# Kernel optimization log

Measured on AMD Instinct MI355X. Metric: run time of the kernel, lower is better.

## Reference

```python
import jax, jax.numpy as jnp
import numpy as np

N_NODES = 100000
N_EDGES = 1600000
D_IN = 64
D_OUT = 64
K_PLUS = 3
ALPHA = 0.5
EXPONENT = -0.25


def _dir_norm_edge_weights(row, col, n, exponent):
    # directed_norm: D_out^exp A D_in^exp, zero-degree -> 0 weight
    ones = jnp.ones(row.shape[0], dtype=jnp.float32)
    out_deg = jax.ops.segment_sum(ones, row, num_segments=n)
    in_deg = jax.ops.segment_sum(ones, col, num_segments=n)
    out_inv = jnp.where(out_deg > 0, jnp.power(jnp.maximum(out_deg, 1.0), exponent), 0.0)
    in_inv = jnp.where(in_deg > 0, jnp.power(jnp.maximum(in_deg, 1.0), exponent), 0.0)
    return out_inv[row] * in_inv[col]


def _spmm(w, x, out_idx, gather_idx, n):
    # y[out_idx] += w * x[gather_idx]
    return jax.ops.segment_sum(w[:, None] * x[gather_idx], out_idx, num_segments=n)


def setup_inputs() -> dict:
    key = jax.random.key(0)
    ks = jax.random.split(key, 7)
    x_real = jax.random.normal(ks[0], (N_NODES, D_IN), dtype=jnp.float32)
    x_imag = jax.random.normal(ks[1], (N_NODES, D_IN), dtype=jnp.float32)
    edge_index = jax.random.randint(ks[2], (2, N_EDGES), 0, N_NODES, dtype=jnp.int32)
    s = 1.0 / np.sqrt(D_IN)
    W_real = jax.random.normal(ks[3], (K_PLUS, D_OUT, D_IN), dtype=jnp.float32) * s
    b_real = jax.random.normal(ks[4], (K_PLUS, D_OUT), dtype=jnp.float32) * s
    W_imag = jax.random.normal(ks[5], (K_PLUS, D_OUT, D_IN), dtype=jnp.float32) * s
    b_imag = jax.random.normal(ks[6], (K_PLUS, D_OUT), dtype=jnp.float32) * s
    return {"x_real": x_real, "x_imag": x_imag, "edge_index": edge_index,
            "W_real": W_real, "b_real": b_real, "W_imag": W_imag, "b_imag": b_imag}


def reference(x_real, x_imag, edge_index, W_real, b_real, W_imag, b_imag):
    n = x_real.shape[0]
    row, col = edge_index[0], edge_index[1]
    # adj_norm edge weights; adj_t_norm weights are identical scalars per edge
    # (in/out degrees swap under transpose), only the scatter direction differs.
    w = _dir_norm_edge_weights(row, col, n, EXPONENT)

    y_real = _spmm(w, x_real, row, col, n)    # adj_norm @ x_real
    y_imag = _spmm(w, x_imag, row, col, n)    # adj_norm @ x_imag
    y_real_t = _spmm(w, x_real, col, row, n)  # adj_t_norm @ x_real
    y_imag_t = _spmm(w, x_imag, col, row, n)  # adj_t_norm @ x_imag

    def lin_r(y):  # [K, N, O] per-order real linear
        return jnp.einsum('nd,kod->kno', y, W_real) + b_real[:, None, :]

    def lin_i(y):
        return jnp.einsum('nd,kod->kno', y, W_imag) + b_imag[:, None, :]

    coeffs = (0.5 ** jnp.arange(K_PLUS, dtype=jnp.float32))[:, None, None]  # exp penalty, i=0 -> 1

    lr_yr, li_yr = lin_r(y_real), lin_i(y_real)
    lr_yi, li_yi = lin_r(y_imag), lin_i(y_imag)
    lr_yrt, li_yrt = lin_r(y_real_t), lin_i(y_real_t)
    lr_yit, li_yit = lin_r(y_imag_t), lin_i(y_imag_t)

    sum_real_s2d = jnp.sum((lr_yr - li_yi) * coeffs, axis=0)
    sum_imag_s2d = jnp.sum((li_yr + lr_yi) * coeffs, axis=0)
    sum_real_d2s = jnp.sum((lr_yrt - li_yit) * coeffs, axis=0)
    # NOTE: faithful to original source, which uses y_real (not y_real_t) here.
    sum_imag_d2s = jnp.sum((li_yr + lr_yit) * coeffs, axis=0)

    total_real = ALPHA * sum_real_s2d + (1.0 - ALPHA) * sum_real_d2s
    total_imag = ALPHA * sum_imag_s2d + (1.0 - ALPHA) * sum_imag_d2s
    return total_real, total_imag
```

## Files before the change

kernel.cpp:

```cpp
#include <hip/hip_runtime.h>
#include <hip/hip_fp16.h>


constexpr int D = 64;
constexpr int GSC = 500;
constexpr int SLOTSZ = 8192;

typedef _Float16 f16x8 __attribute__((ext_vector_type(8)));
typedef float f32x4 __attribute__((ext_vector_type(4)));

__device__ __forceinline__ float2 h2_to_f2(uint p) {
  __half2 h = *(__half2*)&p;
  return __half22float2(h);
}

__global__ __launch_bounds__(1024) void prep_kernel(
    const float* __restrict__ Wr, const float* __restrict__ br,
    const float* __restrict__ Wi, const float* __restrict__ bi,
    uint4* __restrict__ Bfrag, float* __restrict__ cR, float* __restrict__ cI,
    int* __restrict__ Ccur, int NBUK) {
  __shared__ uint sWh[4096];
  int t = threadIdx.x;
  for (int i = t; i < 4096; i += 1024) {
    int o = i >> 6, d = i & 63;
    float wr = Wr[i] + 0.5f * Wr[4096 + i] + 0.25f * Wr[8192 + i];
    float wi = Wi[i] + 0.5f * Wi[4096 + i] + 0.25f * Wi[8192 + i];
    __half2 h = __floats2half2_rn(wr, wi);
    sWh[d * 64 + o] = *(uint*)&h;
  }
  if (t < 64) {
    float brv = br[t] + 0.5f * br[64 + t] + 0.25f * br[128 + t];
    float biv = bi[t] + 0.5f * bi[64 + t] + 0.25f * bi[128 + t];
    cR[t] = brv - biv;
    cI[t] = brv + biv;
  }
  for (int i = t; i < 2 * NBUK; i += 1024) {
    int b = (i < NBUK) ? i : (i - NBUK);
    Ccur[i << 4] = b * SLOTSZ;
  }
  __syncthreads();
  for (int tt = t; tt < 2048; tt += 1024) {
    int ln = tt & 63, fr = tt >> 6;
    int mat = fr >> 4, kt = (fr >> 2) & 3, nt = fr & 3;
    int o = (ln & 15) + 16 * nt;
    int k0 = 8 * (ln >> 4) + 32 * kt;
    uint wbits[4];
#pragma unroll
    for (int jj = 0; jj < 4; ++jj) {
      float vv[2];
#pragma unroll
      for (int s = 0; s < 2; ++s) {
        int k = k0 + 2 * jj + s;
        float2 wrwi = h2_to_f2(sWh[(k & 63) * 64 + o]);
        vv[s] = (k < 64) ? wrwi.x : (mat ? wrwi.y : -wrwi.y);
      }
      __half2 hh = __floats2half2_rn(vv[0], vv[1]);
      wbits[jj] = *(uint*)&hh;
    }
    Bfrag[tt] = make_uint4(wbits[0], wbits[1], wbits[2], wbits[3]);
  }
}

__global__ __launch_bounds__(256) void part_scatter(
    const int* __restrict__ row, const int* __restrict__ col,
    int* __restrict__ Ccur,
    uint* __restrict__ pout, uint* __restrict__ pin, int E, int NBUK, int CH) {
  __shared__ int co[512], ci[512];
  int t = threadIdx.x, g = blockIdx.x;
  co[t] = 0;
  co[t + 256] = 0;
  ci[t] = 0;
  ci[t + 256] = 0;
  __syncthreads();
  int e0 = g * CH, e1 = min(E, e0 + CH);
  int g0 = e0 >> 2, g1 = (e1 + 3) >> 2;
  for (int gi = g0 + t; gi < g1; gi += 256) {
    int4 r4 = ((const int4*)row)[gi];
    int4 c4 = ((const int4*)col)[gi];
    atomicAdd(&co[r4.x >> 8], 1);
    atomicAdd(&co[r4.y >> 8], 1);
    atomicAdd(&co[r4.z >> 8], 1);
    atomicAdd(&co[r4.w >> 8], 1);
    atomicAdd(&ci[c4.x >> 8], 1);
    atomicAdd(&ci[c4.y >> 8], 1);
    atomicAdd(&ci[c4.z >> 8], 1);
    atomicAdd(&ci[c4.w >> 8], 1);
  }
  __syncthreads();
  for (int i = t; i < NBUK; i += 256) {
    int c = co[i];
    co[i] = c ? atomicAdd(&Ccur[i << 4], c) : 0;
    c = ci[i];
    ci[i] = c ? atomicAdd(&Ccur[(NBUK + i) << 4], c) : 0;
  }
  __syncthreads();
  for (int gi = g0 + t; gi < g1; gi += 256) {
    int4 r4 = ((const int4*)row)[gi];
    int4 c4 = ((const int4*)col)[gi];
#define SCAT1(R, C)                                          \
  {                                                          \
    int po = atomicAdd(&co[(R) >> 8], 1);                    \
    pout[po] = ((uint)((R) & 255) << 17) | (uint)(C);        \
    int pi = atomicAdd(&ci[(C) >> 8], 1);                    \
    pin[pi] = ((uint)((C) & 255) << 17) | (uint)(R);         \
  }
    SCAT1(r4.x, c4.x);
    SCAT1(r4.y, c4.y);
    SCAT1(r4.z, c4.z);
    SCAT1(r4.w, c4.w);
#undef SCAT1
  }
}

__global__ __launch_bounds__(256) void build_kernel(
    const uint* __restrict__ pout, const uint* __restrict__ pin,
    const int* __restrict__ Ccur,
    int2* __restrict__ ofsp_out, int2* __restrict__ ofsp_in,
    float* __restrict__ inv_out, float* __restrict__ inv_in,
    uint* __restrict__ idx_out, uint* __restrict__ idx_in, int NBUK, int N) {
  const uint* p = blockIdx.y ? pin : pout;
  int2* ofsp = blockIdx.y ? ofsp_in : ofsp_out;
  float* inv = blockIdx.y ? inv_in : inv_out;
  uint* idx = blockIdx.y ? idx_in : idx_out;
  __shared__ int ld[256], cur[256];
  __shared__ int ws[4];
  int t = threadIdx.x, b = blockIdx.x;
  ld[t] = 0;
  __syncthreads();
  int s = b * SLOTSZ;
  int e = Ccur[((blockIdx.y ? NBUK : 0) + b) << 4];
  int j = s + t;
  for (; j + 768 < e; j += 1024) {
    uint p0 = p[j], p1 = p[j + 256], p2 = p[j + 512], p3 = p[j + 768];
    atomicAdd(&ld[p0 >> 17], 1);
    atomicAdd(&ld[p1 >> 17], 1);
    atomicAdd(&ld[p2 >> 17], 1);
    atomicAdd(&ld[p3 >> 17], 1);
  }
  for (; j < e; j += 256) atomicAdd(&ld[p[j] >> 17], 1);
  __syncthreads();
  int d = ld[t];
  int lane = t & 63, wv = t >> 6, sc = d;
#pragma unroll
  for (int off = 1; off < 64; off <<= 1) {
    int u = __shfl_up(sc, off);
    if (lane >= off) sc += u;
  }
  if (lane == 63) ws[wv] = sc;
  __syncthreads();
  int wbase = 0;
#pragma unroll
  for (int w = 0; w < 4; ++w)
    if (w < wv) wbase += ws[w];
  int start = s + wbase + sc - d;
  cur[t] = start;
  int n = (b << 8) + t;
  if (n < N) {
    ofsp[n] = make_int2(start, start + d);
    inv[n] = d ? rsqrtf(sqrtf((float)d)) : 0.0f;
  }
  __syncthreads();
  j = s + t;
#define FILL1(PK)                                  \
  {                                                \
    int pos = atomicAdd(&cur[(PK) >> 17], 1);      \
    idx[pos] = (PK) & 0x1FFFFu;                    \
  }
  for (; j + 768 < e; j += 1024) {
    uint p0 = p[j], p1 = p[j + 256], p2 = p[j + 512], p3 = p[j + 768];
    FILL1(p0);
    FILL1(p1);
    FILL1(p2);
    FILL1(p3);
  }
  for (; j < e; j += 256) {
    uint pk = p[j];
    FILL1(pk);
  }
#undef FILL1
}


__global__ void pack_kernel(const float* __restrict__ xr, const float* __restrict__ xi,
                            uint* __restrict__ xp, int total4) {
  int i = blockIdx.x * blockDim.x + threadIdx.x;
  if (i < total4) {
    float4 a = ((const float4*)xr)[i];
    float4 b = ((const float4*)xi)[i];
    __half2 h;
    uint4 o;
    h = __floats2half2_rn(a.x, b.x); o.x = *(uint*)&h;
    h = __floats2half2_rn(a.y, b.y); o.y = *(uint*)&h;
    h = __floats2half2_rn(a.z, b.z); o.z = *(uint*)&h;
    h = __floats2half2_rn(a.w, b.w); o.w = *(uint*)&h;
    ((uint4*)xp)[i] = o;
  }
}

__global__ __launch_bounds__(256) void gather_kernel(
    const uint4* __restrict__ xp4,
    const uint* __restrict__ idx_out, const uint* __restrict__ idx_in,
    const int2* __restrict__ ofsp_out, const int2* __restrict__ ofsp_in,
    const float* __restrict__ inv_out, const float* __restrict__ inv_in,
    uint* __restrict__ Apack, int N) {
  int wv = threadIdx.x >> 6;
  int lane = threadIdx.x & 63;
  int sub = lane >> 4;
  int q = lane & 15;
  int wid = blockIdx.x * 4 + wv;
  int nw = gridDim.x * 4;
  for (int n = wid; n < N; n += nw) {
    float4 u1 = {0, 0, 0, 0}, s1 = {0, 0, 0, 0};
    float4 v2 = {0, 0, 0, 0}, s2 = {0, 0, 0, 0};
#define ACC(P, SC, U, S)                                                \
  {                                                                     \
    float2 a0 = h2_to_f2((P).x), a1 = h2_to_f2((P).y);                  \
    float2 a2 = h2_to_f2((P).z), a3 = h2_to_f2((P).w);                  \
    U.x += SC * a0.x; S.x += SC * a0.y; U.y += SC * a1.x; S.y += SC * a1.y; \
    U.z += SC * a2.x; S.z += SC * a2.y; U.w += SC * a3.x; S.w += SC * a3.y; \
  }
    {
      int2 se = ofsp_out[n];
      int lo = se.x, hi = se.y;
      int len8 = (hi - lo) & ~7;
      int j = lo;
      for (; j < lo + len8; j += 8) {
        uint e0 = idx_out[j + sub];
        uint e1 = idx_out[j + 4 + sub];
        uint4 p0 = xp4[(size_t)e0 * 16 + q];
        uint4 p1 = xp4[(size_t)e1 * 16 + q];
        float sc0 = inv_in[e0], sc1 = inv_in[e1];
        ACC(p0, sc0, u1, s1);
        ACC(p1, sc1, u1, s1);
      }
      for (; j < hi; j += 4) {
        if (j + sub < hi) {
          uint e0 = idx_out[j + sub];
          uint4 p0 = xp4[(size_t)e0 * 16 + q];
          float sc0 = inv_in[e0];
          ACC(p0, sc0, u1, s1);
        }
      }
    }
    {
      int2 se = ofsp_in[n];
      int lo = se.x, hi = se.y;
      int len8 = (hi - lo) & ~7;
      int j = lo;
      for (; j < lo + len8; j += 8) {
        uint e0 = idx_in[j + sub];
        uint e1 = idx_in[j + 4 + sub];
        uint4 p0 = xp4[(size_t)e0 * 16 + q];
        uint4 p1 = xp4[(size_t)e1 * 16 + q];
        float sc0 = inv_out[e0], sc1 = inv_out[e1];
        ACC(p0, sc0, v2, s2);
        ACC(p1, sc1, v2, s2);
      }
      for (; j < hi; j += 4) {
        if (j + sub < hi) {
          uint e0 = idx_in[j + sub];
          uint4 p0 = xp4[(size_t)e0 * 16 + q];
          float sc0 = inv_out[e0];
          ACC(p0, sc0, v2, s2);
        }
      }
    }
#undef ACC
#pragma unroll
    for (int m = 16; m < 64; m <<= 1) {
      u1.x += __shfl_xor(u1.x, m); u1.y += __shfl_xor(u1.y, m);
      u1.z += __shfl_xor(u1.z, m); u1.w += __shfl_xor(u1.w, m);
      s1.x += __shfl_xor(s1.x, m); s1.y += __shfl_xor(s1.y, m);
      s1.z += __shfl_xor(s1.z, m); s1.w += __shfl_xor(s1.w, m);
      v2.x += __shfl_xor(v2.x, m); v2.y += __shfl_xor(v2.y, m);
      v2.z += __shfl_xor(v2.z, m); v2.w += __shfl_xor(v2.w, m);
      s2.x += __shfl_xor(s2.x, m); s2.y += __shfl_xor(s2.y, m);
      s2.z += __shfl_xor(s2.z, m); s2.w += __shfl_xor(s2.w, m);
    }
    if (sub == 0) {
      float io = inv_out[n], ii = inv_in[n];
      float4 uu = make_float4(io * u1.x, io * u1.y, io * u1.z, io * u1.w);
      float4 vv = make_float4(ii * v2.x, ii * v2.y, ii * v2.z, ii * v2.w);
      float4 ss = make_float4(io * s1.x + ii * s2.x, io * s1.y + ii * s2.y,
                              io * s1.z + ii * s2.z, io * s1.w + ii * s2.w);
      uint* base = Apack + (size_t)n * 96 + 2 * q;
      __half2 h;
      uint2 w;
      h = __floats2half2_rn(0.5f * (uu.x + vv.x), 0.5f * (uu.y + vv.y)); w.x = *(uint*)&h;
      h = __floats2half2_rn(0.5f * (uu.z + vv.z), 0.5f * (uu.w + vv.w)); w.y = *(uint*)&h;
      *(uint2*)base = w;
      h = __floats2half2_rn(0.5f * ss.x, 0.5f * ss.y); w.x = *(uint*)&h;
      h = __floats2half2_rn(0.5f * ss.z, 0.5f * ss.w); w.y = *(uint*)&h;
      *(uint2*)(base + 32) = w;
      h = __floats2half2_rn(uu.x, uu.y); w.x = *(uint*)&h;
      h = __floats2half2_rn(uu.z, uu.w); w.y = *(uint*)&h;
      *(uint2*)(base + 64) = w;
    }
  }
}

__global__ __launch_bounds__(256) void gemm_kernel(
    const ushort* __restrict__ Apack, const uint4* __restrict__ Bfrag,
    const float* __restrict__ cR, const float* __restrict__ cI,
    float* __restrict__ out_real, float* __restrict__ out_imag, int N) {
  __shared__ uint4 sB[2048];
  for (int i = threadIdx.x; i < 2048; i += 256) sB[i] = Bfrag[i];
  __syncthreads();
  int lane = threadIdx.x & 63, wv = threadIdx.x >> 6;
  int l15 = lane & 15, l4 = lane >> 4;
  float bR[4], bI[4];
#pragma unroll
  for (int nt = 0; nt < 4; ++nt) {
    bR[nt] = cR[l15 + 16 * nt];
    bI[nt] = cI[l15 + 16 * nt];
  }
  int tiles = (N + 15) >> 4;
  int gw = blockIdx.x * 4 + wv, nw = gridDim.x * 4;
  for (int tt = gw; tt < tiles; tt += nw) {
    int n0 = tt << 4;
    int arow = min(n0 + l15, N - 1);
    const ushort* ap = Apack + (size_t)arow * 192 + 8 * l4;
    f16x8 a[6];
#pragma unroll
    for (int kt = 0; kt < 6; ++kt) a[kt] = *(const f16x8*)(ap + 32 * kt);
    f32x4 cr[4], ci[4];
#pragma unroll
    for (int nt = 0; nt < 4; ++nt) {
      cr[nt] = (f32x4){0.f, 0.f, 0.f, 0.f};
      ci[nt] = (f32x4){0.f, 0.f, 0.f, 0.f};
    }
#pragma unroll
    for (int kt = 0; kt < 4; ++kt) {
#pragma unroll
      for (int nt = 0; nt < 4; ++nt) {
        f16x8 b0 = *(const f16x8*)&sB[(kt * 4 + nt) * 64 + lane];
        cr[nt] = __builtin_amdgcn_mfma_f32_16x16x32_f16(a[kt], b0, cr[nt], 0, 0, 0);
        f16x8 b1 = *(const f16x8*)&sB[(16 + kt * 4 + nt) * 64 + lane];
        ci[nt] = __builtin_amdgcn_mfma_f32_16x16x32_f16(a[kt + 2], b1, ci[nt], 0, 0, 0);
      }
    }
#pragma unroll
    for (int nt = 0; nt < 4; ++nt) {
#pragma unroll
      for (int r = 0; r < 4; ++r) {
        int node = n0 + 4 * l4 + r;
        if (node < N) {
          out_real[(size_t)node * 64 + l15 + 16 * nt] = cr[nt][r] + bR[nt];
          out_imag[(size_t)node * 64 + l15 + 16 * nt] = ci[nt][r] + bI[nt];
        }
      }
    }
  }
}

extern "C" void kernel_launch(void* const* d_in, const int* in_sizes, int n_in,
                              void* d_out, int out_size, void* d_ws, size_t ws_size,
                              hipStream_t stream) {
  const float* x_real = (const float*)d_in[0];
  const float* x_imag = (const float*)d_in[1];
  const int* edge = (const int*)d_in[2];
  const float* W_real = (const float*)d_in[3];
  const float* b_real = (const float*)d_in[4];
  const float* W_imag = (const float*)d_in[5];
  const float* b_imag = (const float*)d_in[6];

  const int N = in_sizes[0] / D;
  const int E = in_sizes[2] / 2;
  const int* row = edge;
  const int* col = edge + E;

  const int NBUK = (N + 255) >> 8;
  const int CH = ((E / GSC + 3) & ~3);
  const size_t SLOTS = (size_t)NBUK * SLOTSZ;

  uint* xp       = (uint*)d_ws;
  uint* idx_out  = xp + (size_t)N * D;
  uint* idx_in   = idx_out + SLOTS;
  uint* Apack    = idx_in + SLOTS;
  uint* pout     = Apack;
  uint* pin      = pout + SLOTS;
  uint4* Bfrag   = (uint4*)(Apack + (size_t)N * 96);
  int* Ccur      = (int*)(Bfrag + 2048);
  int2* ofsp_out = (int2*)(Ccur + 2 * NBUK * 16);
  int2* ofsp_in  = ofsp_out + N;
  float* inv_out = (float*)(ofsp_in + N);
  float* inv_in  = inv_out + N;
  float* cR      = inv_in + N;
  float* cI      = cR + 64;

  float* out_real = (float*)d_out;
  float* out_imag = out_real + (size_t)N * D;

  prep_kernel<<<1, 1024, 0, stream>>>(W_real, b_real, W_imag, b_imag,
                                      Bfrag, cR, cI, Ccur, NBUK);

  pack_kernel<<<(N * 16 + 255) / 256, 256, 0, stream>>>(x_real, x_imag, xp, N * 16);

  part_scatter<<<GSC, 256, 0, stream>>>(row, col, Ccur, pout, pin, E, NBUK, CH);

  build_kernel<<<dim3(NBUK, 2), 256, 0, stream>>>(pout, pin, Ccur,
                                                  ofsp_out, ofsp_in,
                                                  inv_out, inv_in,
                                                  idx_out, idx_in, NBUK, N);

  gather_kernel<<<4096, 256, 0, stream>>>((const uint4*)xp, idx_out, idx_in,
                                          ofsp_out, ofsp_in, inv_out, inv_in,
                                          Apack, N);
  gemm_kernel<<<1568, 256, 0, stream>>>((const ushort*)Apack, Bfrag, cR, cI,
                                        out_real, out_imag, N);
}
```

Measured before the change: 331.3 us.

## Fuse prep/pack/scatter kernels and embed neighbor scale into edge index

Merges weight prep, fp16 packing and the partition scatter into one heterogeneous launch, with Ccur zeroed by a memset and bucket-relative counters. The build step is split into an offsets kernel and a fill kernel. The fill kernel stores each neighbor's fp16 inverse-degree scale in the upper bits of the index word, so the gather no longer does a separate random load of inv_in/inv_out per edge. The cost is one extra kernel launch, a random scale lookup moved into the fill pass, and fp16 precision for the edge scales.

```diff
diff --git a/kernel.cpp b/kernel.cpp
--- a/kernel.cpp
+++ b/kernel.cpp
@@ -5,6 +5,7 @@
 constexpr int D = 64;
 constexpr int GSC = 500;
 constexpr int SLOTSZ = 8192;
+constexpr int PREPB = 8;
 
 typedef _Float16 f16x8 __attribute__((ext_vector_type(8)));
 typedef float f32x4 __attribute__((ext_vector_type(4)));
@@ -14,89 +15,50 @@
   return __half22float2(h);
 }
 
-__global__ __launch_bounds__(1024) void prep_kernel(
+__global__ __launch_bounds__(256) void phase1_kernel(
+    const int* __restrict__ row, const int* __restrict__ col,
+    int* __restrict__ Ccur, uint* __restrict__ pout, uint* __restrict__ pin,
+    const float* __restrict__ xr, const float* __restrict__ xi,
+    uint* __restrict__ xp,
     const float* __restrict__ Wr, const float* __restrict__ br,
     const float* __restrict__ Wi, const float* __restrict__ bi,
     uint4* __restrict__ Bfrag, float* __restrict__ cR, float* __restrict__ cI,
-    int* __restrict__ Ccur, int NBUK) {
-  __shared__ uint sWh[4096];
-  int t = threadIdx.x;
-  for (int i = t; i < 4096; i += 1024) {
-    int o = i >> 6, d = i & 63;
-    float wr = Wr[i] + 0.5f * Wr[4096 + i] + 0.25f * Wr[8192 + i];
-    float wi = Wi[i] + 0.5f * Wi[4096 + i] + 0.25f * Wi[8192 + i];
-    __half2 h = __floats2half2_rn(wr, wi);
-    sWh[d * 64 + o] = *(uint*)&h;
-  }
-  if (t < 64) {
-    float brv = br[t] + 0.5f * br[64 + t] + 0.25f * br[128 + t];
-    float biv = bi[t] + 0.5f * bi[64 + t] + 0.25f * bi[128 + t];
-    cR[t] = brv - biv;
-    cI[t] = brv + biv;
-  }
-  for (int i = t; i < 2 * NBUK; i += 1024) {
-    int b = (i < NBUK) ? i : (i - NBUK);
-    Ccur[i << 4] = b * SLOTSZ;
-  }
-  __syncthreads();
-  for (int tt = t; tt < 2048; tt += 1024) {
-    int ln = tt & 63, fr = tt >> 6;
-    int mat = fr >> 4, kt = (fr >> 2) & 3, nt = fr & 3;
-    int o = (ln & 15) + 16 * nt;
-    int k0 = 8 * (ln >> 4) + 32 * kt;
-    uint wbits[4];
-#pragma unroll
-    for (int jj = 0; jj < 4; ++jj) {
-      float vv[2];
-#pragma unroll
-      for (int s = 0; s < 2; ++s) {
-        int k = k0 + 2 * jj + s;
-        float2 wrwi = h2_to_f2(sWh[(k & 63) * 64 + o]);
-        vv[s] = (k < 64) ? wrwi.x : (mat ? wrwi.y : -wrwi.y);
-      }
-      __half2 hh = __floats2half2_rn(vv[0], vv[1]);
-      wbits[jj] = *(uint*)&hh;
-    }
-    Bfrag[tt] = make_uint4(wbits[0], wbits[1], wbits[2], wbits[3]);
-  }
-}
-
-__global__ __launch_bounds__(256) void part_scatter(
-    const int* __restrict__ row, const int* __restrict__ col,
-    int* __restrict__ Ccur,
-    uint* __restrict__ pout, uint* __restrict__ pin, int E, int NBUK, int CH) {
-  __shared__ int co[512], ci[512];
-  int t = threadIdx.x, g = blockIdx.x;
-  co[t] = 0;
-  co[t + 256] = 0;
-  ci[t] = 0;
-  ci[t + 256] = 0;
-  __syncthreads();
-  int e0 = g * CH, e1 = min(E, e0 + CH);
-  int g0 = e0 >> 2, g1 = (e1 + 3) >> 2;
-  for (int gi = g0 + t; gi < g1; gi += 256) {
-    int4 r4 = ((const int4*)row)[gi];
-    int4 c4 = ((const int4*)col)[gi];
-    atomicAdd(&co[r4.x >> 8], 1);
-    atomicAdd(&co[r4.y >> 8], 1);
-    atomicAdd(&co[r4.z >> 8], 1);
-    atomicAdd(&co[r4.w >> 8], 1);
-    atomicAdd(&ci[c4.x >> 8], 1);
-    atomicAdd(&ci[c4.y >> 8], 1);
-    atomicAdd(&ci[c4.z >> 8], 1);
-    atomicAdd(&ci[c4.w >> 8], 1);
-  }
-  __syncthreads();
-  for (int i = t; i < NBUK; i += 256) {
-    int c = co[i];
-    co[i] = c ? atomicAdd(&Ccur[i << 4], c) : 0;
-    c = ci[i];
-    ci[i] = c ? atomicAdd(&Ccur[(NBUK + i) << 4], c) : 0;
-  }
-  __syncthreads();
-  for (int gi = g0 + t; gi < g1; gi += 256) {
-    int4 r4 = ((const int4*)row)[gi];
-    int4 c4 = ((const int4*)col)[gi];
+    int E, int NBUK, int CH, int NPACK, int total4) {
+  __shared__ uint smem[4096];
+  int t = threadIdx.x, bid = blockIdx.x;
+  if (bid < GSC) {
+    int* co = (int*)smem;
+    int* ci = co + 512;
+    co[t] = 0;
+    co[t + 256] = 0;
+    ci[t] = 0;
+    ci[t + 256] = 0;
+    __syncthreads();
+    int e0 = bid * CH, e1 = min(E, e0 + CH);
+    int g0 = e0 >> 2, g1 = (e1 + 3) >> 2;
+    for (int gi = g0 + t; gi < g1; gi += 256) {
+      int4 r4 = ((const int4*)row)[gi];
+      int4 c4 = ((const int4*)col)[gi];
+      atomicAdd(&co[r4.x >> 8], 1);
+      atomicAdd(&co[r4.y >> 8], 1);
+      atomicAdd(&co[r4.z >> 8], 1);
+      atomicAdd(&co[r4.w >> 8], 1);
+      atomicAdd(&ci[c4.x >> 8], 1);
+      atomicAdd(&ci[c4.y >> 8], 1);
+      atomicAdd(&ci[c4.z >> 8], 1);
+      atomicAdd(&ci[c4.w >> 8], 1);
+    }
+    __syncthreads();
+    for (int i = t; i < NBUK; i += 256) {
+      int c = co[i];
+      co[i] = c ? i * SLOTSZ + atomicAdd(&Ccur[i << 4], c) : 0;
+      c = ci[i];
+      ci[i] = c ? i * SLOTSZ + atomicAdd(&Ccur[(NBUK + i) << 4], c) : 0;
+    }
+    __syncthreads();
+    for (int gi = g0 + t; gi < g1; gi += 256) {
+      int4 r4 = ((const int4*)row)[gi];
+      int4 c4 = ((const int4*)col)[gi];
 #define SCAT1(R, C)                                          \
   {                                                          \
     int po = atomicAdd(&co[(R) >> 8], 1);                    \
@@ -104,31 +66,80 @@
     int pi = atomicAdd(&ci[(C) >> 8], 1);                    \
     pin[pi] = ((uint)((C) & 255) << 17) | (uint)(R);         \
   }
-    SCAT1(r4.x, c4.x);
-    SCAT1(r4.y, c4.y);
-    SCAT1(r4.z, c4.z);
-    SCAT1(r4.w, c4.w);
+      SCAT1(r4.x, c4.x);
+      SCAT1(r4.y, c4.y);
+      SCAT1(r4.z, c4.z);
+      SCAT1(r4.w, c4.w);
 #undef SCAT1
-  }
-}
-
-__global__ __launch_bounds__(256) void build_kernel(
+    }
+  } else if (bid < GSC + NPACK) {
+    int i = (bid - GSC) * 256 + t;
+    if (i < total4) {
+      float4 a = ((const float4*)xr)[i];
+      float4 b = ((const float4*)xi)[i];
+      __half2 h;
+      uint4 o;
+      h = __floats2half2_rn(a.x, b.x); o.x = *(uint*)&h;
+      h = __floats2half2_rn(a.y, b.y); o.y = *(uint*)&h;
+      h = __floats2half2_rn(a.z, b.z); o.z = *(uint*)&h;
+      h = __floats2half2_rn(a.w, b.w); o.w = *(uint*)&h;
+      ((uint4*)xp)[i] = o;
+    }
+  } else {
+    int pb = bid - GSC - NPACK;
+    uint* sWh = smem;
+    for (int i = t; i < 4096; i += 256) {
+      int o = i >> 6, d = i & 63;
+      float wr = Wr[i] + 0.5f * Wr[4096 + i] + 0.25f * Wr[8192 + i];
+      float wi = Wi[i] + 0.5f * Wi[4096 + i] + 0.25f * Wi[8192 + i];
+      __half2 h = __floats2half2_rn(wr, wi);
+      sWh[d * 64 + o] = *(uint*)&h;
+    }
+    if (pb == 0 && t < 64) {
+      float brv = br[t] + 0.5f * br[64 + t] + 0.25f * br[128 + t];
+      float biv = bi[t] + 0.5f * bi[64 + t] + 0.25f * bi[128 + t];
+      cR[t] = brv - biv;
+      cI[t] = brv + biv;
+    }
+    __syncthreads();
+    int tt = pb * 256 + t;
+    int ln = tt & 63, fr = tt >> 6;
+    int mat = fr >> 4, kt = (fr >> 2) & 3, nt = fr & 3;
+    int o = (ln & 15) + 16 * nt;
+    int k0 = 8 * (ln >> 4) + 32 * kt;
+    uint wbits[4];
+#pragma unroll
+    for (int jj = 0; jj < 4; ++jj) {
+      float vv[2];
+#pragma unroll
+      for (int s = 0; s < 2; ++s) {
+        int k = k0 + 2 * jj + s;
+        float2 wrwi = h2_to_f2(sWh[(k & 63) * 64 + o]);
+        vv[s] = (k < 64) ? wrwi.x : (mat ? wrwi.y : -wrwi.y);
+      }
+      __half2 hh = __floats2half2_rn(vv[0], vv[1]);
+      wbits[jj] = *(uint*)&hh;
+    }
+    Bfrag[tt] = make_uint4(wbits[0], wbits[1], wbits[2], wbits[3]);
+  }
+}
+
+__global__ __launch_bounds__(256) void offsets_kernel(
     const uint* __restrict__ pout, const uint* __restrict__ pin,
     const int* __restrict__ Ccur,
     int2* __restrict__ ofsp_out, int2* __restrict__ ofsp_in,
     float* __restrict__ inv_out, float* __restrict__ inv_in,
-    uint* __restrict__ idx_out, uint* __restrict__ idx_in, int NBUK, int N) {
+    int NBUK, int N) {
   const uint* p = blockIdx.y ? pin : pout;
   int2* ofsp = blockIdx.y ? ofsp_in : ofsp_out;
   float* inv = blockIdx.y ? inv_in : inv_out;
-  uint* idx = blockIdx.y ? idx_in : idx_out;
-  __shared__ int ld[256], cur[256];
+  __shared__ int ld[256];
   __shared__ int ws[4];
   int t = threadIdx.x, b = blockIdx.x;
   ld[t] = 0;
   __syncthreads();
   int s = b * SLOTSZ;
-  int e = Ccur[((blockIdx.y ? NBUK : 0) + b) << 4];
+  int e = s + Ccur[((blockIdx.y ? NBUK : 0) + b) << 4];
   int j = s + t;
   for (; j + 768 < e; j += 1024) {
     uint p0 = p[j], p1 = p[j + 256], p2 = p[j + 512], p3 = p[j + 768];
@@ -153,19 +164,38 @@
   for (int w = 0; w < 4; ++w)
     if (w < wv) wbase += ws[w];
   int start = s + wbase + sc - d;
-  cur[t] = start;
   int n = (b << 8) + t;
   if (n < N) {
     ofsp[n] = make_int2(start, start + d);
     inv[n] = d ? rsqrtf(sqrtf((float)d)) : 0.0f;
   }
+}
+
+__global__ __launch_bounds__(256) void bucket_fill(
+    const uint* __restrict__ pout, const uint* __restrict__ pin,
+    const int* __restrict__ Ccur,
+    const int2* __restrict__ ofsp_out, const int2* __restrict__ ofsp_in,
+    const float* __restrict__ inv_out, const float* __restrict__ inv_in,
+    uint* __restrict__ idx_out, uint* __restrict__ idx_in, int NBUK, int N) {
+  const uint* p = blockIdx.y ? pin : pout;
+  const int2* ofsp = blockIdx.y ? ofsp_in : ofsp_out;
+  const float* invnb = blockIdx.y ? inv_out : inv_in;
+  uint* idx = blockIdx.y ? idx_in : idx_out;
+  __shared__ int cur[256];
+  int t = threadIdx.x, b = blockIdx.x;
+  int n = (b << 8) + t;
+  cur[t] = (n < N) ? ofsp[n].x : 0;
   __syncthreads();
-  j = s + t;
-#define FILL1(PK)                                  \
-  {                                                \
-    int pos = atomicAdd(&cur[(PK) >> 17], 1);      \
-    idx[pos] = (PK) & 0x1FFFFu;                    \
-  }
+  int s = b * SLOTSZ;
+  int e = s + Ccur[((blockIdx.y ? NBUK : 0) + b) << 4];
+#define FILL1(PK)                                                       \
+  {                                                                     \
+    uint nbr = (PK) & 0x1FFFFu;                                         \
+    uint hb = (uint)__half_as_ushort(__float2half(invnb[nbr]));         \
+    int pos = atomicAdd(&cur[(PK) >> 17], 1);                           \
+    idx[pos] = (hb << 17) | nbr;                                        \
+  }
+  int j = s + t;
   for (; j + 768 < e; j += 1024) {
     uint p0 = p[j], p1 = p[j + 256], p2 = p[j + 512], p3 = p[j + 768];
     FILL1(p0);
@@ -178,23 +208,6 @@
     FILL1(pk);
   }
 #undef FILL1
-}
-
-
-__global__ void pack_kernel(const float* __restrict__ xr, const float* __restrict__ xi,
-                            uint* __restrict__ xp, int total4) {
-  int i = blockIdx.x * blockDim.x + threadIdx.x;
-  if (i < total4) {
-    float4 a = ((const float4*)xr)[i];
-    float4 b = ((const float4*)xi)[i];
-    __half2 h;
-    uint4 o;
-    h = __floats2half2_rn(a.x, b.x); o.x = *(uint*)&h;
-    h = __floats2half2_rn(a.y, b.y); o.y = *(uint*)&h;
-    h = __floats2half2_rn(a.z, b.z); o.z = *(uint*)&h;
-    h = __floats2half2_rn(a.w, b.w); o.w = *(uint*)&h;
-    ((uint4*)xp)[i] = o;
-  }
 }
 
 __global__ __launch_bounds__(256) void gather_kernel(
@@ -219,6 +232,7 @@
     U.x += SC * a0.x; S.x += SC * a0.y; U.y += SC * a1.x; S.y += SC * a1.y; \
     U.z += SC * a2.x; S.z += SC * a2.y; U.w += SC * a3.x; S.w += SC * a3.y; \
   }
+#define DEC(E) __half2float(__ushort_as_half((ushort)((E) >> 17)))
     {
       int2 se = ofsp_out[n];
       int lo = se.x, hi = se.y;
@@ -227,17 +241,17 @@
       for (; j < lo + len8; j += 8) {
         uint e0 = idx_out[j + sub];
         uint e1 = idx_out[j + 4 + sub];
-        uint4 p0 = xp4[(size_t)e0 * 16 + q];
-        uint4 p1 = xp4[(size_t)e1 * 16 + q];
-        float sc0 = inv_in[e0], sc1 = inv_in[e1];
+        uint4 p0 = xp4[(size_t)(e0 & 0x1FFFFu) * 16 + q];
+        uint4 p1 = xp4[(size_t)(e1 & 0x1FFFFu) * 16 + q];
+        float sc0 = DEC(e0), sc1 = DEC(e1);
         ACC(p0, sc0, u1, s1);
         ACC(p1, sc1, u1, s1);
       }
       for (; j < hi; j += 4) {
         if (j + sub < hi) {
           uint e0 = idx_out[j + sub];
-          uint4 p0 = xp4[(size_t)e0 * 16 + q];
-          float sc0 = inv_in[e0];
+          uint4 p0 = xp4[(size_t)(e0 & 0x1FFFFu) * 16 + q];
+          float sc0 = DEC(e0);
           ACC(p0, sc0, u1, s1);
         }
       }
@@ -250,22 +264,23 @@
       for (; j < lo + len8; j += 8) {
         uint e0 = idx_in[j + sub];
         uint e1 = idx_in[j + 4 + sub];
-        uint4 p0 = xp4[(size_t)e0 * 16 + q];
-        uint4 p1 = xp4[(size_t)e1 * 16 + q];
-        float sc0 = inv_out[e0], sc1 = inv_out[e1];
+        uint4 p0 = xp4[(size_t)(e0 & 0x1FFFFu) * 16 + q];
+        uint4 p1 = xp4[(size_t)(e1 & 0x1FFFFu) * 16 + q];
+        float sc0 = DEC(e0), sc1 = DEC(e1);
         ACC(p0, sc0, v2, s2);
         ACC(p1, sc1, v2, s2);
       }
       for (; j < hi; j += 4) {
         if (j + sub < hi) {
           uint e0 = idx_in[j + sub];
-          uint4 p0 = xp4[(size_t)e0 * 16 + q];
-          float sc0 = inv_out[e0];
+          uint4 p0 = xp4[(size_t)(e0 & 0x1FFFFu) * 16 + q];
+          float sc0 = DEC(e0);
           ACC(p0, sc0, v2, s2);
         }
       }
     }
 #undef ACC
+#undef DEC
 #pragma unroll
     for (int m = 16; m < 64; m <<= 1) {
       u1.x += __shfl_xor(u1.x, m); u1.y += __shfl_xor(u1.y, m);
@@ -371,6 +386,7 @@
 
   const int NBUK = (N + 255) >> 8;
   const int CH = ((E / GSC + 3) & ~3);
+  const int NPACK = (N * 16 + 255) / 256;
   const size_t SLOTS = (size_t)NBUK * SLOTSZ;
 
   uint* xp       = (uint*)d_ws;
@@ -391,17 +407,20 @@
   float* out_real = (float*)d_out;
   float* out_imag = out_real + (size_t)N * D;
 
-  prep_kernel<<<1, 1024, 0, stream>>>(W_real, b_real, W_imag, b_imag,
-                                      Bfrag, cR, cI, Ccur, NBUK);
-
-  pack_kernel<<<(N * 16 + 255) / 256, 256, 0, stream>>>(x_real, x_imag, xp, N * 16);
-
-  part_scatter<<<GSC, 256, 0, stream>>>(row, col, Ccur, pout, pin, E, NBUK, CH);
-
-  build_kernel<<<dim3(NBUK, 2), 256, 0, stream>>>(pout, pin, Ccur,
-                                                  ofsp_out, ofsp_in,
-                                                  inv_out, inv_in,
-                                                  idx_out, idx_in, NBUK, N);
+  hipMemsetAsync(Ccur, 0, 2 * NBUK * 16 * sizeof(int), stream);
+  phase1_kernel<<<GSC + NPACK + PREPB, 256, 0, stream>>>(
+      row, col, Ccur, pout, pin, x_real, x_imag, xp,
+      W_real, b_real, W_imag, b_imag, Bfrag, cR, cI,
+      E, NBUK, CH, NPACK, N * 16);
+
+  offsets_kernel<<<dim3(NBUK, 2), 256, 0, stream>>>(pout, pin, Ccur,
+                                                    ofsp_out, ofsp_in,
+                                                    inv_out, inv_in, NBUK, N);
+
+  bucket_fill<<<dim3(NBUK, 2), 256, 0, stream>>>(pout, pin, Ccur,
+                                                 ofsp_out, ofsp_in,
+                                                 inv_out, inv_in,
+                                                 idx_out, idx_in, NBUK, N);
 
   gather_kernel<<<4096, 256, 0, stream>>>((const uint4*)xp, idx_out, idx_in,
                                           ofsp_out, ofsp_in, inv_out, inv_in,
```

After: 330.5 us. Within noise of the previous version (-0.2%).
